# Kernel optimization log

Measured on AMD Instinct MI355X. Metric: run time of the kernel, lower is better.

## Reference

```python
import jax, jax.numpy as jnp
import numpy as np

B, S, D = 4, 4096, 1024
ROT = 4          # rotation_dim (quaternion)
MAX_SEQ = 4096   # max_seq_len
EPS = 1e-5


def setup_inputs() -> dict:
    key = jax.random.key(0)
    k_x, = jax.random.split(key, 1)
    x = jax.random.normal(k_x, (B, S, D), dtype=jnp.float32)
    # Learned parameters (torch inits: eye, ones, LN gamma=1 beta=0)
    rotation_matrix = jnp.eye(ROT, dtype=jnp.float32)
    frequency_kernel = jnp.ones((MAX_SEQ,), dtype=jnp.float32)
    ln_gamma = jnp.ones((D,), dtype=jnp.float32)
    ln_beta = jnp.zeros((D,), dtype=jnp.float32)
    return {"x": x, "rotation_matrix": rotation_matrix,
            "frequency_kernel": frequency_kernel,
            "ln_gamma": ln_gamma, "ln_beta": ln_beta}


def reference(x, rotation_matrix, frequency_kernel, ln_gamma, ln_beta):
    b, s, d = x.shape
    quat_dim = d // ROT
    # (b, s, quat_dim, 4)
    x_quat = x.reshape(b, s, quat_dim, ROT)
    # FFT along sequence axis, multiply by (real) learnable frequency kernel
    x_freq = jnp.fft.fft(x_quat, axis=1)
    kernel = frequency_kernel[:s].reshape(1, s, 1, 1)
    filtered_time = jnp.fft.ifft(x_freq * kernel, axis=1).real.astype(x.dtype)
    # Small 4x4 quaternion rotation applied to the last axis
    rotated = jnp.einsum('bstq,oq->bsto', filtered_time, rotation_matrix)
    out = rotated.reshape(b, s, d)
    # LayerNorm over the feature dim
    mean = jnp.mean(out, axis=-1, keepdims=True)
    var = jnp.var(out, axis=-1, keepdims=True)
    out = (out - mean) * jax.lax.rsqrt(var + EPS) * ln_gamma + ln_beta
    return out
```

## Files before the change

### kernel.cpp

```cpp
#include <hip/hip_runtime.h>
#include <hip/hip_bf16.h>
#include <hip/hip_fp16.h>

#define NB 4
#define NS 4096
#define ND 1024
#define NP 512
#define LN_EPS 1e-5f

__device__ __forceinline__ int pad(int i) { return i + (i >> 4); }

__device__ __forceinline__ float2 cadd(float2 a, float2 b) { return make_float2(a.x + b.x, a.y + b.y); }
__device__ __forceinline__ float2 csub(float2 a, float2 b) { return make_float2(a.x - b.x, a.y - b.y); }
__device__ __forceinline__ float2 cmul(float2 a, float2 b) {
  return make_float2(a.x * b.x - a.y * b.y, a.x * b.y + a.y * b.x);
}
__device__ __forceinline__ float2 cmulc(float2 a, float2 b) {
  return make_float2(a.x * b.x + a.y * b.y, a.y * b.x - a.x * b.y);
}
__device__ __forceinline__ unsigned short f2bf(float f) {
  unsigned int u = __float_as_uint(f);
  u += 0x7FFFu + ((u >> 16) & 1u);
  return (unsigned short)(u >> 16);
}
__device__ __forceinline__ float bf2f(unsigned int lo16) {
  return __uint_as_float(lo16 << 16);
}
__device__ __forceinline__ unsigned int packbf(float a, float b) {
  return (unsigned int)f2bf(a) | ((unsigned int)f2bf(b) << 16);
}
__device__ __forceinline__ unsigned int pkh(float2 v) {
  __half2 h = __floats2half2_rn(v.x, v.y);
  return *reinterpret_cast<unsigned int*>(&h);
}
__device__ __forceinline__ float2 uph(unsigned int u) {
  __half2 h = *reinterpret_cast<__half2*>(&u);
  return __half22float2(h);
}

__device__ __forceinline__ int rev12(int p) {
  return ((p & 15) << 8) | (p & 240) | (p >> 8);
}

template<int S>
__device__ __forceinline__ void dft16(float2* x) {
  const float C1 = 0.9238795325112867f, S1 = 0.3826834323650898f, RT = 0.7071067811865476f;
  const float WC[10] = {1.f, C1, RT, S1, 0.f, -S1, -RT, -C1, -1.f, -C1};
  const float WS[10] = {0.f, S1, RT, C1, 1.f, C1,  RT,  S1,  0.f, -S1};
  #pragma unroll
  for (int m0 = 0; m0 < 4; ++m0) {
    float2 a = x[m0], b = x[m0 + 4], c = x[m0 + 8], d = x[m0 + 12];
    float2 t0 = cadd(a, c), t1 = csub(a, c), t2 = cadd(b, d), t3 = csub(b, d);
    float2 t3i = (S < 0) ? make_float2(t3.y, -t3.x) : make_float2(-t3.y, t3.x);
    x[m0]      = cadd(t0, t2);
    x[m0 + 4]  = cadd(t1, t3i);
    x[m0 + 8]  = csub(t0, t2);
    x[m0 + 12] = csub(t1, t3i);
  }
  #pragma unroll
  for (int r0 = 1; r0 < 4; ++r0)
    #pragma unroll
    for (int m0 = 1; m0 < 4; ++m0) {
      const int k = m0 * r0;
      const float2 w = make_float2(WC[k], (S < 0) ? -WS[k] : WS[k]);
      x[m0 + 4 * r0] = cmul(x[m0 + 4 * r0], w);
    }
  float2 y[16];
  #pragma unroll
  for (int r0 = 0; r0 < 4; ++r0) {
    float2 a = x[4 * r0], b = x[4 * r0 + 1], c = x[4 * r0 + 2], d = x[4 * r0 + 3];
    float2 t0 = cadd(a, c), t1 = csub(a, c), t2 = cadd(b, d), t3 = csub(b, d);
    float2 t3i = (S < 0) ? make_float2(t3.y, -t3.x) : make_float2(-t3.y, t3.x);
    y[r0]      = cadd(t0, t2);
    y[r0 + 4]  = cadd(t1, t3i);
    y[r0 + 8]  = csub(t0, t2);
    y[r0 + 12] = csub(t1, t3i);
  }
  #pragma unroll
  for (int i = 0; i < 16; ++i) x[i] = y[i];
}

__global__ void kprep(const float* __restrict__ fk, float* __restrict__ fkp,
                      float2* __restrict__ TwA, float2* __restrict__ TwC) {
  const int p = blockIdx.x * 256 + threadIdx.x;
  fkp[p] = fk[rev12(p)] * (1.0f / 4096.0f);
  const float TPON = 1.5339807878856412e-3f;
  if (p < 256) {
    const int a = p >> 4, r = p & 15;
    float sn, cs;
    __sincosf((float)(a * r) * (TPON * 16.f), &sn, &cs);
    TwA[p] = make_float2(cs, -sn);
    __sincosf((float)(a * r) * TPON, &sn, &cs);
    TwC[p] = make_float2(cs, -sn);
  }
}

__global__ __launch_bounds__(256) void ktransP(const float* __restrict__ x,
                                               unsigned int* __restrict__ xP) {
  __shared__ float tile[64][65];
  const int b = blockIdx.z;
  const int s0 = blockIdx.x * 64;
  const int d0 = blockIdx.y * 64;
  const int t = threadIdx.x;
  const float* xb = x + (size_t)b * NS * ND;
  #pragma unroll
  for (int p = 0; p < 4; ++p) {
    int r = (t >> 4) + p * 16;
    int c = (t & 15) * 4;
    float4 v = *reinterpret_cast<const float4*>(xb + (size_t)(s0 + r) * ND + (d0 + c));
    tile[r][c] = v.x; tile[r][c + 1] = v.y; tile[r][c + 2] = v.z; tile[r][c + 3] = v.w;
  }
  __syncthreads();
  const int pl = t >> 3;
  const int sc0 = (t & 7) * 8;
  unsigned int buf[8];
  #pragma unroll
  for (int j = 0; j < 8; ++j)
    buf[j] = packbf(tile[sc0 + j][2 * pl], tile[sc0 + j][2 * pl + 1]);
  unsigned int* dst = xP + (size_t)((b * NP) + (d0 >> 1) + pl) * NS + s0 + sc0;
  *reinterpret_cast<uint4*>(dst)     = make_uint4(buf[0], buf[1], buf[2], buf[3]);
  *reinterpret_cast<uint4*>(dst + 4) = make_uint4(buf[4], buf[5], buf[6], buf[7]);
}

__global__ __launch_bounds__(512, 4) void kfft(unsigned int* __restrict__ xP,
                                               const float* __restrict__ fkp,
                                               const float2* __restrict__ TwAg,
                                               const float2* __restrict__ TwCg,
                                               const float* __restrict__ R) {
  extern __shared__ unsigned char smem[];
  unsigned int* zdyn = (unsigned int*)smem;
  float2* twl = (float2*)(smem + 34816);
  const int t = threadIdx.x;
  const int h = t >> 8;
  const int tt = t & 255;
  const int q = blockIdx.x;
  const int b = blockIdx.y;
  const unsigned int* rowP = xP + (size_t)(b * NP + q * 2 + h) * NS;
  unsigned int* zz = zdyn + (size_t)h * 4352;
  const int ta = tt >> 4, tc = tt & 15;
  float2 x[16];

  twl[t] = (t < 256) ? TwAg[t] : TwCg[t - 256];

  #pragma unroll
  for (int m = 0; m < 16; ++m) {
    unsigned int u = rowP[tt + 256 * m];
    x[m] = make_float2(bf2f(u & 0xffffu), bf2f(u >> 16));
  }
  dft16<-1>(x);
  __syncthreads();
  zz[pad(tt)] = pkh(x[0]);
  #pragma unroll
  for (int r = 1; r < 16; ++r) {
    float2 tw = cmul(twl[r * 16 + ta], twl[256 + r * 16 + tc]);
    zz[pad(tt + 256 * r)] = pkh(cmul(x[r], tw));
  }
  __syncthreads();
  {
    const int bs = 256 * (tt >> 4) + (tt & 15);
    const int j = tt & 15;
    #pragma unroll
    for (int m = 0; m < 16; ++m) x[m] = uph(zz[pad(bs + 16 * m)]);
    dft16<-1>(x);
    zz[pad(bs)] = pkh(x[0]);
    #pragma unroll
    for (int r = 1; r < 16; ++r) zz[pad(bs + 16 * r)] = pkh(cmul(x[r], twl[r * 16 + j]));
  }
  __syncthreads();
  {
    const int bs = 16 * tt;
    #pragma unroll
    for (int m = 0; m < 16; ++m) x[m] = uph(zz[pad(bs + m)]);
    dft16<-1>(x);
    #pragma unroll
    for (int r4 = 0; r4 < 4; ++r4) {
      float4 kv = *reinterpret_cast<const float4*>(fkp + bs + 4 * r4);
      x[4 * r4 + 0].x *= kv.x; x[4 * r4 + 0].y *= kv.x;
      x[4 * r4 + 1].x *= kv.y; x[4 * r4 + 1].y *= kv.y;
      x[4 * r4 + 2].x *= kv.z; x[4 * r4 + 2].y *= kv.z;
      x[4 * r4 + 3].x *= kv.w; x[4 * r4 + 3].y *= kv.w;
    }
    dft16<1>(x);
    #pragma unroll
    for (int r = 0; r < 16; ++r) zz[pad(bs + r)] = pkh(x[r]);
  }
  __syncthreads();
  {
    const int bs = 256 * (tt >> 4) + (tt & 15);
    const int j = tt & 15;
    x[0] = uph(zz[pad(bs)]);
    #pragma unroll
    for (int m = 1; m < 16; ++m) x[m] = cmulc(uph(zz[pad(bs + 16 * m)]), twl[m * 16 + j]);
    dft16<1>(x);
    #pragma unroll
    for (int r = 0; r < 16; ++r) zz[pad(bs + 16 * r)] = pkh(x[r]);
  }
  __syncthreads();
  {
    x[0] = uph(zz[pad(tt)]);
    #pragma unroll
    for (int m = 1; m < 16; ++m)
      x[m] = cmulc(cmulc(uph(zz[pad(tt + 256 * m)]), twl[m * 16 + ta]), twl[256 + m * 16 + tc]);
    dft16<1>(x);
    #pragma unroll
    for (int r = 0; r < 16; ++r) zz[pad(tt + 256 * r)] = pkh(x[r]);
  }
  __syncthreads();
  const float r00 = R[0],  r01 = R[1],  r02 = R[2],  r03 = R[3];
  const float r10 = R[4],  r11 = R[5],  r12 = R[6],  r13 = R[7];
  const float r20 = R[8],  r21 = R[9],  r22 = R[10], r23 = R[11];
  const float r30 = R[12], r31 = R[13], r32 = R[14], r33 = R[15];
  unsigned int* row0 = xP + (size_t)(b * NP + q * 2) * NS;
  unsigned int* row1 = row0 + NS;
  #pragma unroll
  for (int k = 0; k < 8; ++k) {
    const int s = t + 512 * k;
    float2 v0 = uph(zdyn[pad(s)]);
    float2 v1 = uph(zdyn[4352 + pad(s)]);
    float c0 = v0.x, c1 = v0.y, c2 = v1.x, c3 = v1.y;
    float o0 = r00 * c0 + r01 * c1 + r02 * c2 + r03 * c3;
    float o1 = r10 * c0 + r11 * c1 + r12 * c2 + r13 * c3;
    float o2 = r20 * c0 + r21 * c1 + r22 * c2 + r23 * c3;
    float o3 = r30 * c0 + r31 * c1 + r32 * c2 + r33 * c3;
    row0[s] = packbf(o0, o1);
    row1[s] = packbf(o2, o3);
  }
}

__global__ __launch_bounds__(256) void kapply2(const unsigned int* __restrict__ xP,
                                               const float* __restrict__ gam,
                                               const float* __restrict__ bet,
                                               float* __restrict__ out) {
  __shared__ float tile[64][65];
  __shared__ float rs[4][64], rq[4][64];
  __shared__ float smean[64], sinv[64];
  const int b = blockIdx.y;
  const int s0 = blockIdx.x * 64;
  const int t = threadIdx.x;
  const int w = t >> 6;
  const int l = t & 63;
  const unsigned int* src = xP + (size_t)b * NP * NS + s0 + l;
  float as = 0.f, aq = 0.f;
  for (int p = w * 4; p < NP; p += 16) {
    #pragma unroll
    for (int j = 0; j < 4; ++j) {
      unsigned int u = src[(size_t)(p + j) * NS];
      float v0 = bf2f(u & 0xffffu), v1 = bf2f(u >> 16);
      as += v0 + v1;
      aq += v0 * v0 + v1 * v1;
    }
  }
  rs[w][l] = as;
  rq[w][l] = aq;
  __syncthreads();
  if (w == 0) {
    float sm = (rs[0][l] + rs[1][l]) + (rs[2][l] + rs[3][l]);
    float sq = (rq[0][l] + rq[1][l]) + (rq[2][l] + rq[3][l]);
    float mean = sm * (1.0f / ND);
    float var = sq * (1.0f / ND) - mean * mean;
    smean[l] = mean;
    sinv[l] = rsqrtf(var + LN_EPS);
  }
  __syncthreads();
  const int pl = t >> 3;
  const int sc0 = (t & 7) * 8;
  for (int c = 0; c < ND / 64; ++c) {
    const int d0 = c * 64;
    const unsigned int* srcc = xP + (size_t)(b * NP + (d0 >> 1) + pl) * NS + s0 + sc0;
    uint4 u0 = *reinterpret_cast<const uint4*>(srcc);
    uint4 u1 = *reinterpret_cast<const uint4*>(srcc + 4);
    const unsigned int uu[8] = {u0.x, u0.y, u0.z, u0.w, u1.x, u1.y, u1.z, u1.w};
    #pragma unroll
    for (int j = 0; j < 8; ++j) {
      tile[2 * pl][sc0 + j]     = bf2f(uu[j] & 0xffffu);
      tile[2 * pl + 1][sc0 + j] = bf2f(uu[j] >> 16);
    }
    __syncthreads();
    float* dst = out + ((size_t)b * NS + s0) * ND + d0;
    #pragma unroll
    for (int p = 0; p < 4; ++p) {
      int sr = (t >> 4) + p * 16;
      float mean = smean[sr];
      float inv = sinv[sr];
      int dc = (t & 15) * 4;
      float4 g4 = *reinterpret_cast<const float4*>(gam + d0 + dc);
      float4 b4 = *reinterpret_cast<const float4*>(bet + d0 + dc);
      float4 o;
      o.x = (tile[dc + 0][sr] - mean) * inv * g4.x + b4.x;
      o.y = (tile[dc + 1][sr] - mean) * inv * g4.y + b4.y;
      o.z = (tile[dc + 2][sr] - mean) * inv * g4.z + b4.z;
      o.w = (tile[dc + 3][sr] - mean) * inv * g4.w + b4.w;
      *reinterpret_cast<float4*>(dst + (size_t)sr * ND + dc) = o;
    }
    __syncthreads();
  }
}

extern "C" void kernel_launch(void* const* d_in, const int* in_sizes, int n_in,
                              void* d_out, int out_size, void* d_ws, size_t ws_size,
                              hipStream_t stream) {
  const float* x  = (const float*)d_in[0];
  const float* R  = (const float*)d_in[1];
  const float* fk = (const float*)d_in[2];
  const float* gm = (const float*)d_in[3];
  const float* bt = (const float*)d_in[4];
  float* out = (float*)d_out;

  char* ws = (char*)d_ws;
  unsigned int* xP = (unsigned int*)ws;
  float*  fkp  = (float*)(ws + (size_t)NB * NP * NS * 4);
  float2* TwA  = (float2*)(fkp + NS);
  float2* TwC  = TwA + 256;

  (void)hipFuncSetAttribute((const void*)kfft,
                            hipFuncAttributeMaxDynamicSharedMemorySize, 38912);

  kprep<<<16, 256, 0, stream>>>(fk, fkp, TwA, TwC);
  ktransP<<<dim3(NS / 64, ND / 64, NB), 256, 0, stream>>>(x, xP);
  kfft<<<dim3(ND / 4, NB), 512, 38912, stream>>>(xP, fkp, TwA, TwC, R);
  kapply2<<<dim3(NS / 64, NB), 256, 0, stream>>>(xP, gm, bt, out);
}
```

Before: 95.36 us.

## Split LayerNorm into separate stats and apply kernels for more parallelism

The fused stats+apply kernel, which ran only 256 blocks each looping over all 16 feature chunks, is split in two. A stats kernel writes per-row sum and sum of squares to workspace, and an apply kernel uses a 3D grid of 16K blocks, each handling one 64x64 tile. This is meant to raise occupancy and memory-level parallelism in the output-writing phase. In exchange it adds a kernel launch and a small round trip of the statistics through global memory, and the stats pass still uses only 256 blocks.

```diff
diff --git a/kernel.cpp b/kernel.cpp
--- a/kernel.cpp
+++ b/kernel.cpp
@@ -227,18 +227,13 @@
   }
 }
 
-__global__ __launch_bounds__(256) void kapply2(const unsigned int* __restrict__ xP,
-                                               const float* __restrict__ gam,
-                                               const float* __restrict__ bet,
-                                               float* __restrict__ out) {
-  __shared__ float tile[64][65];
-  __shared__ float rs[4][64], rq[4][64];
-  __shared__ float smean[64], sinv[64];
+__global__ __launch_bounds__(256) void kstatsP(const unsigned int* __restrict__ xP,
+                                               float* __restrict__ ssum,
+                                               float* __restrict__ ssq) {
   const int b = blockIdx.y;
   const int s0 = blockIdx.x * 64;
-  const int t = threadIdx.x;
-  const int w = t >> 6;
-  const int l = t & 63;
+  const int w = threadIdx.x >> 6;
+  const int l = threadIdx.x & 63;
   const unsigned int* src = xP + (size_t)b * NP * NS + s0 + l;
   float as = 0.f, aq = 0.f;
   for (int p = w * 4; p < NP; p += 16) {
@@ -250,49 +245,56 @@
       aq += v0 * v0 + v1 * v1;
     }
   }
+  __shared__ float rs[4][64], rq[4][64];
   rs[w][l] = as;
   rq[w][l] = aq;
   __syncthreads();
   if (w == 0) {
-    float sm = (rs[0][l] + rs[1][l]) + (rs[2][l] + rs[3][l]);
-    float sq = (rq[0][l] + rq[1][l]) + (rq[2][l] + rq[3][l]);
-    float mean = sm * (1.0f / ND);
-    float var = sq * (1.0f / ND) - mean * mean;
-    smean[l] = mean;
-    sinv[l] = rsqrtf(var + LN_EPS);
-  }
-  __syncthreads();
+    ssum[b * NS + s0 + l] = (rs[0][l] + rs[1][l]) + (rs[2][l] + rs[3][l]);
+    ssq[b * NS + s0 + l]  = (rq[0][l] + rq[1][l]) + (rq[2][l] + rq[3][l]);
+  }
+}
+
+__global__ __launch_bounds__(256) void kapplyP(const unsigned int* __restrict__ xP,
+                                               const float* __restrict__ ssum,
+                                               const float* __restrict__ ssq,
+                                               const float* __restrict__ gam,
+                                               const float* __restrict__ bet,
+                                               float* __restrict__ out) {
+  __shared__ float tile[64][65];
+  const int b = blockIdx.z;
+  const int s0 = blockIdx.x * 64;
+  const int d0 = blockIdx.y * 64;
+  const int t = threadIdx.x;
   const int pl = t >> 3;
   const int sc0 = (t & 7) * 8;
-  for (int c = 0; c < ND / 64; ++c) {
-    const int d0 = c * 64;
-    const unsigned int* srcc = xP + (size_t)(b * NP + (d0 >> 1) + pl) * NS + s0 + sc0;
-    uint4 u0 = *reinterpret_cast<const uint4*>(srcc);
-    uint4 u1 = *reinterpret_cast<const uint4*>(srcc + 4);
-    const unsigned int uu[8] = {u0.x, u0.y, u0.z, u0.w, u1.x, u1.y, u1.z, u1.w};
-    #pragma unroll
-    for (int j = 0; j < 8; ++j) {
-      tile[2 * pl][sc0 + j]     = bf2f(uu[j] & 0xffffu);
-      tile[2 * pl + 1][sc0 + j] = bf2f(uu[j] >> 16);
-    }
-    __syncthreads();
-    float* dst = out + ((size_t)b * NS + s0) * ND + d0;
-    #pragma unroll
-    for (int p = 0; p < 4; ++p) {
-      int sr = (t >> 4) + p * 16;
-      float mean = smean[sr];
-      float inv = sinv[sr];
-      int dc = (t & 15) * 4;
-      float4 g4 = *reinterpret_cast<const float4*>(gam + d0 + dc);
-      float4 b4 = *reinterpret_cast<const float4*>(bet + d0 + dc);
-      float4 o;
-      o.x = (tile[dc + 0][sr] - mean) * inv * g4.x + b4.x;
-      o.y = (tile[dc + 1][sr] - mean) * inv * g4.y + b4.y;
-      o.z = (tile[dc + 2][sr] - mean) * inv * g4.z + b4.z;
-      o.w = (tile[dc + 3][sr] - mean) * inv * g4.w + b4.w;
-      *reinterpret_cast<float4*>(dst + (size_t)sr * ND + dc) = o;
-    }
-    __syncthreads();
+  const unsigned int* src = xP + (size_t)(b * NP + (d0 >> 1) + pl) * NS + s0 + sc0;
+  uint4 u0 = *reinterpret_cast<const uint4*>(src);
+  uint4 u1 = *reinterpret_cast<const uint4*>(src + 4);
+  const unsigned int uu[8] = {u0.x, u0.y, u0.z, u0.w, u1.x, u1.y, u1.z, u1.w};
+  #pragma unroll
+  for (int j = 0; j < 8; ++j) {
+    tile[2 * pl][sc0 + j]     = bf2f(uu[j] & 0xffffu);
+    tile[2 * pl + 1][sc0 + j] = bf2f(uu[j] >> 16);
+  }
+  __syncthreads();
+  float* dst = out + ((size_t)b * NS + s0) * ND + d0;
+  #pragma unroll
+  for (int p = 0; p < 4; ++p) {
+    int sr = (t >> 4) + p * 16;
+    int s = s0 + sr;
+    float mean = ssum[b * NS + s] * (1.0f / ND);
+    float var = ssq[b * NS + s] * (1.0f / ND) - mean * mean;
+    float inv = rsqrtf(var + LN_EPS);
+    int dc = (t & 15) * 4;
+    float4 g4 = *reinterpret_cast<const float4*>(gam + d0 + dc);
+    float4 b4 = *reinterpret_cast<const float4*>(bet + d0 + dc);
+    float4 o;
+    o.x = (tile[dc + 0][sr] - mean) * inv * g4.x + b4.x;
+    o.y = (tile[dc + 1][sr] - mean) * inv * g4.y + b4.y;
+    o.z = (tile[dc + 2][sr] - mean) * inv * g4.z + b4.z;
+    o.w = (tile[dc + 3][sr] - mean) * inv * g4.w + b4.w;
+    *reinterpret_cast<float4*>(dst + (size_t)sr * ND + dc) = o;
   }
 }
 
@@ -308,7 +310,9 @@
 
   char* ws = (char*)d_ws;
   unsigned int* xP = (unsigned int*)ws;
-  float*  fkp  = (float*)(ws + (size_t)NB * NP * NS * 4);
+  float*  ssum = (float*)(ws + (size_t)NB * NP * NS * 4);
+  float*  ssq  = ssum + NB * NS;
+  float*  fkp  = ssq + NB * NS;
   float2* TwA  = (float2*)(fkp + NS);
   float2* TwC  = TwA + 256;
 
@@ -318,5 +322,6 @@
   kprep<<<16, 256, 0, stream>>>(fk, fkp, TwA, TwC);
   ktransP<<<dim3(NS / 64, ND / 64, NB), 256, 0, stream>>>(x, xP);
   kfft<<<dim3(ND / 4, NB), 512, 38912, stream>>>(xP, fkp, TwA, TwC, R);
-  kapply2<<<dim3(NS / 64, NB), 256, 0, stream>>>(xP, gm, bt, out);
-}
+  kstatsP<<<dim3(NS / 64, NB), 256, 0, stream>>>(xP, ssum, ssq);
+  kapplyP<<<dim3(NS / 64, ND / 64, NB), 256, 0, stream>>>(xP, ssum, ssq, gm, bt, out);
+}
```

After: 95.37 us. No clear change (+0.0%).
